# Performance work log

Measured on AMD Instinct MI355X. Metric: run time of the kernel, lower is better.

## Reference

```python
import jax, jax.numpy as jnp
import numpy as np
import math

B, E, N = 32, 256, 64
KV_DIM, Q_DIM = 100, 768


def setup_inputs() -> dict:
    key = jax.random.key(0)
    ks = jax.random.split(key, 8)
    q = jax.random.normal(ks[0], (B, Q_DIM), dtype=jnp.float32)
    k = jax.random.normal(ks[1], (B, E, N, KV_DIM), dtype=jnp.float32)
    v = jax.random.normal(ks[2], (B, E, N, KV_DIM), dtype=jnp.float32)
    input_ent = jax.random.randint(ks[3], (B, E), 0, 50000)
    # xavier-uniform-initialized weights (torch Linear: y = x @ W.T + b)
    def xavier(k_, fan_out, fan_in):
        lim = math.sqrt(6.0 / (fan_in + fan_out))
        return jax.random.uniform(k_, (fan_out, fan_in), jnp.float32, -lim, lim)
    W_q = xavier(ks[4], KV_DIM, Q_DIM)
    b_q = jnp.zeros((KV_DIM,), jnp.float32)
    W_kv = xavier(ks[5], KV_DIM, KV_DIM)
    W_v = xavier(ks[6], KV_DIM, KV_DIM)
    return {"input_ent": input_ent, "q": q, "k": k, "v": v,
            "W_q": W_q, "b_q": b_q, "W_kv": W_kv, "W_v": W_v}


def reference(input_ent, q, k, v, W_q, b_q, W_kv, W_v):
    # mode == 'candidate_pos', graphsage=False -> output = self_attention(q, k, v)
    # Q projection + tanh: [B, Kv]
    Qp = jnp.tanh(q @ W_q.T + b_q)
    # K projection: [B, E, N, Kv]
    Kp = k @ W_kv.T
    # broadcasted dot-product score: [B, E, N]
    att = jnp.einsum('bd,bend->ben', Qp, Kp) / math.sqrt(KV_DIM)
    # masked_fill(att == 0, -10000)
    att = jnp.where(att == 0.0, jnp.float32(-10000.0), att)
    # LeakyReLU (default negative_slope=0.01) then softmax over neighbor dim
    att = jax.nn.softmax(jax.nn.leaky_relu(att, 0.01), axis=2)
    # masked_fill(att == 1/N, 0)
    att = jnp.where(att == jnp.float32(1.0 / N), jnp.float32(0.0), att)
    # V projection and weighted aggregation over neighbors: [B, E, Kv]
    Vp = v @ W_v.T
    return jnp.einsum('ben,bend->bed', att, Vp)
```

## Files before the change

### kernel.cpp

```cpp
#include <hip/hip_runtime.h>

#define B 32
#define E 256
#define N 64
#define KV 100
#define QD 768

__global__ __launch_bounds__(256) void prep_kernel(
    const float* __restrict__ q,
    const float* __restrict__ W_q,
    const float* __restrict__ b_q,
    const float* __restrict__ W_kv,
    const float* __restrict__ W_v,
    float* __restrict__ Qk,
    float* __restrict__ W_vT)
{
    const int blk = blockIdx.x;
    const int tid = threadIdx.x;

    if (blk == B) {
        for (int idx = tid; idx < KV * KV; idx += 256) {
            int d = idx / KV, i = idx % KV;
            W_vT[idx] = W_v[i * KV + d];
        }
        return;
    }

    __shared__ float q_lds[QD];
    __shared__ float Qp_lds[KV];
    const int b = blk;

    for (int i = tid; i < QD; i += 256) q_lds[i] = q[b * QD + i];
    __syncthreads();

    const int i = tid >> 1, h = tid & 1;
    if (i < KV) {
        float acc = 0.f;
        const float* wrow = W_q + i * QD + h * (QD / 2);
        const float* qrow = q_lds + h * (QD / 2);
        #pragma unroll 8
        for (int d = 0; d < QD / 2; d++) acc += qrow[d] * wrow[d];
        acc += __shfl_xor(acc, 1);
        if (h == 0) Qp_lds[i] = tanhf(acc + b_q[i]);
    }
    __syncthreads();

    if (tid < KV) {
        float acc = 0.f;
        #pragma unroll 4
        for (int ii = 0; ii < KV; ii++) acc += Qp_lds[ii] * W_kv[ii * KV + tid];
        Qk[b * KV + tid] = acc * 0.1f;
    }
}

__global__ __launch_bounds__(256) void attn_kernel(
    const float* __restrict__ k,
    const float* __restrict__ v,
    const float* __restrict__ Qk,
    const float* __restrict__ W_vT,
    float* __restrict__ out)
{
    __shared__ float att_lds[N];
    __shared__ float part_lds[2][KV];
    __shared__ float agg_lds[KV];

    const int tid = threadIdx.x;
    const int be  = blockIdx.x;
    const int b   = be >> 8;

    {
        const int n = tid >> 2, sub = tid & 3;
        const float4* krow = (const float4*)(k + (size_t)be * (N * KV) + n * KV);
        const float4* qk4  = (const float4*)(Qk + b * KV);
        float acc = 0.f;
        #pragma unroll
        for (int j = sub; j < KV / 4; j += 4) {
            float4 kk = krow[j];
            float4 qq = qk4[j];
            acc += qq.x * kk.x + qq.y * kk.y + qq.z * kk.z + qq.w * kk.w;
        }
        acc += __shfl_xor(acc, 1);
        acc += __shfl_xor(acc, 2);
        if (sub == 0) {
            float a = acc;
            if (a == 0.0f) a = -10000.0f;
            a = (a > 0.0f) ? a : 0.01f * a;
            att_lds[n] = a;
        }
    }
    __syncthreads();

    if (tid < 64) {
        float x = att_lds[tid];
        float m = x;
        #pragma unroll
        for (int o = 32; o; o >>= 1) m = fmaxf(m, __shfl_xor(m, o));
        float e = __expf(x - m);
        float s = e;
        #pragma unroll
        for (int o = 32; o; o >>= 1) s += __shfl_xor(s, o);
        float r = e / s;
        if (r == 0.015625f) r = 0.0f;
        att_lds[tid] = r;
    }
    __syncthreads();

    if (tid < 200) {
        const int half = tid / 100;
        const int d    = tid - half * 100;
        const float* vcol = v + (size_t)be * (N * KV) + d;
        float a = 0.f;
        #pragma unroll
        for (int i = 0; i < 32; i++) {
            int nn = half * 32 + i;
            a += att_lds[nn] * vcol[(size_t)nn * KV];
        }
        part_lds[half][d] = a;
    }
    __syncthreads();

    if (tid < KV) agg_lds[tid] = part_lds[0][tid] + part_lds[1][tid];
    __syncthreads();

    if (tid < KV) {
        float acc = 0.f;
        #pragma unroll 4
        for (int d = 0; d < KV; d++)
            acc += agg_lds[d] * W_vT[d * KV + tid];
        out[(size_t)be * KV + tid] = acc;
    }
}

extern "C" void kernel_launch(void* const* d_in, const int* in_sizes, int n_in,
                              void* d_out, int out_size, void* d_ws, size_t ws_size,
                              hipStream_t stream) {
    const float* q    = (const float*)d_in[1];
    const float* k    = (const float*)d_in[2];
    const float* v    = (const float*)d_in[3];
    const float* W_q  = (const float*)d_in[4];
    const float* b_q  = (const float*)d_in[5];
    const float* W_kv = (const float*)d_in[6];
    const float* W_v  = (const float*)d_in[7];
    float* out  = (float*)d_out;

    float* Qk   = (float*)d_ws;
    float* W_vT = Qk + B * KV;

    prep_kernel<<<B + 1, 256, 0, stream>>>(q, W_q, b_q, W_kv, W_v, Qk, W_vT);
    attn_kernel<<<B * E, 256, 0, stream>>>(k, v, Qk, W_vT, out);
}
```

Baseline: 113.6 us.

## Split attention into score and aggregation kernels with vectorized V loads

Splits the fused attention kernel into a score kernel that streams K and writes raw scores to workspace, and an aggregation kernel. The aggregation kernel issues its float4 V register loads before the softmax so the V fetch overlaps the score reads and the reduction. The final projection now reads W_v rows directly as float4, which removes the W_v transpose from the prep kernel. This adds a third launch and a round trip of the score array through global memory.

```diff
diff --git a/kernel.cpp b/kernel.cpp
--- a/kernel.cpp
+++ b/kernel.cpp
@@ -11,24 +11,13 @@
     const float* __restrict__ W_q,
     const float* __restrict__ b_q,
     const float* __restrict__ W_kv,
-    const float* __restrict__ W_v,
-    float* __restrict__ Qk,
-    float* __restrict__ W_vT)
+    float* __restrict__ Qk)
 {
-    const int blk = blockIdx.x;
     const int tid = threadIdx.x;
-
-    if (blk == B) {
-        for (int idx = tid; idx < KV * KV; idx += 256) {
-            int d = idx / KV, i = idx % KV;
-            W_vT[idx] = W_v[i * KV + d];
-        }
-        return;
-    }
+    const int b   = blockIdx.x;
 
     __shared__ float q_lds[QD];
     __shared__ float Qp_lds[KV];
-    const int b = blk;
 
     for (int i = tid; i < QD; i += 256) q_lds[i] = q[b * QD + i];
     __syncthreads();
@@ -53,45 +42,62 @@
     }
 }
 
-__global__ __launch_bounds__(256) void attn_kernel(
+__global__ __launch_bounds__(256) void score_kernel(
     const float* __restrict__ k,
+    const float* __restrict__ Qk,
+    float* __restrict__ att_raw)
+{
+    const int tid  = threadIdx.x;
+    const int quad = tid >> 2, sub = tid & 3;
+    const int r    = blockIdx.x * 64 + quad;
+    const int b    = r >> 14;
+
+    const float4* krow = (const float4*)(k + (size_t)r * KV);
+    const float4* qk4  = (const float4*)(Qk + b * KV);
+
+    float acc = 0.f;
+    #pragma unroll
+    for (int j = sub; j < KV / 4; j += 4) {
+        float4 kk = krow[j];
+        float4 qq = qk4[j];
+        acc += qq.x * kk.x + qq.y * kk.y + qq.z * kk.z + qq.w * kk.w;
+    }
+    acc += __shfl_xor(acc, 1);
+    acc += __shfl_xor(acc, 2);
+    if (sub == 0) {
+        float a = acc;
+        if (a == 0.0f) a = -10000.0f;
+        a = (a > 0.0f) ? a : 0.01f * a;
+        att_raw[r] = a;
+    }
+}
+
+__global__ __launch_bounds__(256) void agg_kernel(
     const float* __restrict__ v,
-    const float* __restrict__ Qk,
-    const float* __restrict__ W_vT,
+    const float* __restrict__ att_raw,
+    const float* __restrict__ W_v,
     float* __restrict__ out)
 {
     __shared__ float att_lds[N];
-    __shared__ float part_lds[2][KV];
-    __shared__ float agg_lds[KV];
+    __shared__ __align__(16) float part_lds[8][KV];
+    __shared__ __align__(16) float agg_lds[KV];
 
     const int tid = threadIdx.x;
     const int be  = blockIdx.x;
-    const int b   = be >> 8;
 
-    {
-        const int n = tid >> 2, sub = tid & 3;
-        const float4* krow = (const float4*)(k + (size_t)be * (N * KV) + n * KV);
-        const float4* qk4  = (const float4*)(Qk + b * KV);
-        float acc = 0.f;
+    const bool active = tid < 200;
+    const int  c  = tid % 25;
+    const int  ng = tid / 25;
+    float4 vr[8];
+    if (active) {
+        const float4* vb = (const float4*)(v + (size_t)be * (N * KV));
         #pragma unroll
-        for (int j = sub; j < KV / 4; j += 4) {
-            float4 kk = krow[j];
-            float4 qq = qk4[j];
-            acc += qq.x * kk.x + qq.y * kk.y + qq.z * kk.z + qq.w * kk.w;
-        }
-        acc += __shfl_xor(acc, 1);
-        acc += __shfl_xor(acc, 2);
-        if (sub == 0) {
-            float a = acc;
-            if (a == 0.0f) a = -10000.0f;
-            a = (a > 0.0f) ? a : 0.01f * a;
-            att_lds[n] = a;
-        }
+        for (int i = 0; i < 8; i++)
+            vr[i] = vb[(ng * 8 + i) * (KV / 4) + c];
     }
-    __syncthreads();
 
     if (tid < 64) {
-        float x = att_lds[tid];
+        float x = att_raw[(size_t)be * N + tid];
         float m = x;
         #pragma unroll
         for (int o = 32; o; o >>= 1) m = fmaxf(m, __shfl_xor(m, o));
@@ -105,29 +111,41 @@
     }
     __syncthreads();
 
-    if (tid < 200) {
-        const int half = tid / 100;
-        const int d    = tid - half * 100;
-        const float* vcol = v + (size_t)be * (N * KV) + d;
-        float a = 0.f;
+    if (active) {
+        float4 a4 = make_float4(0.f, 0.f, 0.f, 0.f);
         #pragma unroll
-        for (int i = 0; i < 32; i++) {
-            int nn = half * 32 + i;
-            a += att_lds[nn] * vcol[(size_t)nn * KV];
+        for (int i = 0; i < 8; i++) {
+            float w = att_lds[ng * 8 + i];
+            a4.x += w * vr[i].x;
+            a4.y += w * vr[i].y;
+            a4.z += w * vr[i].z;
+            a4.w += w * vr[i].w;
         }
-        part_lds[half][d] = a;
+        *(float4*)&part_lds[ng][c * 4] = a4;
     }
     __syncthreads();
 
-    if (tid < KV) agg_lds[tid] = part_lds[0][tid] + part_lds[1][tid];
+    if (tid < KV) {
+        float s = 0.f;
+        #pragma unroll
+        for (int g = 0; g < 8; g++) s += part_lds[g][tid];
+        agg_lds[tid] = s;
+    }
     __syncthreads();
 
-    if (tid < KV) {
+    const int p = tid >> 1, h = tid & 1;
+    if (p < KV) {
+        const float4* wrow = (const float4*)(W_v + p * KV);
+        const float4* a4   = (const float4*)agg_lds;
         float acc = 0.f;
-        #pragma unroll 4
-        for (int d = 0; d < KV; d++)
-            acc += agg_lds[d] * W_vT[d * KV + tid];
-        out[(size_t)be * KV + tid] = acc;
+        #pragma unroll
+        for (int j = h; j < KV / 4; j += 2) {
+            float4 w = wrow[j];
+            float4 a = a4[j];
+            acc += w.x * a.x + w.y * a.y + w.z * a.z + w.w * a.w;
+        }
+        acc += __shfl_xor(acc, 1);
+        if (h == 0) out[(size_t)be * KV + p] = acc;
     }
 }
 
@@ -143,9 +161,10 @@
     const float* W_v  = (const float*)d_in[7];
     float* out  = (float*)d_out;
 
-    float* Qk   = (float*)d_ws;
-    float* W_vT = Qk + B * KV;
+    float* Qk      = (float*)d_ws;
+    float* att_raw = Qk + B * KV;
 
-    prep_kernel<<<B + 1, 256, 0, stream>>>(q, W_q, b_q, W_kv, W_v, Qk, W_vT);
-    attn_kernel<<<B * E, 256, 0, stream>>>(k, v, Qk, W_vT, out);
+    prep_kernel<<<B, 256, 0, stream>>>(q, W_q, b_q, W_kv, Qk);
+    score_kernel<<<(B * E * N) / 64, 256, 0, stream>>>(k, Qk, att_raw);
+    agg_kernel<<<B * E, 256, 0, stream>>>(v, att_raw, W_v, out);
 }
```

New measurement: 144.6 us. 1.27x slower.

## Map one (b,e) attention row per wavefront and drop block barriers

Applied to the files above, without the earlier changes.

Restructures the attention kernel so each 64-lane wavefront handles one (b,e) pair, with four pairs per block. All __syncthreads are removed, and softmax is computed directly in registers from per-lane row dot products. The V aggregation now uses float4 loads with a parity split combined by shuffle. The output projection reads W_v rows with float4 directly, which removes the transpose work in the prep kernel. The trade-off is that per-lane K row reads are strided (each lane reads its own 400-byte row), which may hurt coalescing, and the loads are serialized within each wave.

```diff
diff --git a/kernel.cpp b/kernel.cpp
--- a/kernel.cpp
+++ b/kernel.cpp
@@ -5,30 +5,20 @@
 #define N 64
 #define KV 100
 #define QD 768
+#define WAVES 4
 
 __global__ __launch_bounds__(256) void prep_kernel(
     const float* __restrict__ q,
     const float* __restrict__ W_q,
     const float* __restrict__ b_q,
     const float* __restrict__ W_kv,
-    const float* __restrict__ W_v,
-    float* __restrict__ Qk,
-    float* __restrict__ W_vT)
+    float* __restrict__ Qk)
 {
-    const int blk = blockIdx.x;
     const int tid = threadIdx.x;
-
-    if (blk == B) {
-        for (int idx = tid; idx < KV * KV; idx += 256) {
-            int d = idx / KV, i = idx % KV;
-            W_vT[idx] = W_v[i * KV + d];
-        }
-        return;
-    }
+    const int b   = blockIdx.x;
 
     __shared__ float q_lds[QD];
     __shared__ float Qp_lds[KV];
-    const int b = blk;
 
     for (int i = tid; i < QD; i += 256) q_lds[i] = q[b * QD + i];
     __syncthreads();
@@ -57,77 +47,93 @@
     const float* __restrict__ k,
     const float* __restrict__ v,
     const float* __restrict__ Qk,
-    const float* __restrict__ W_vT,
+    const float* __restrict__ W_v,
     float* __restrict__ out)
 {
-    __shared__ float att_lds[N];
-    __shared__ float part_lds[2][KV];
-    __shared__ float agg_lds[KV];
+    __shared__ __align__(16) float qk_lds[WAVES][KV];
+    __shared__ float att_lds[WAVES][N];
+    __shared__ __align__(16) float agg_lds[WAVES][KV];
 
-    const int tid = threadIdx.x;
-    const int be  = blockIdx.x;
-    const int b   = be >> 8;
+    const int tid  = threadIdx.x;
+    const int wid  = tid >> 6;
+    const int lane = tid & 63;
+    const int be   = blockIdx.x * WAVES + wid;
+    const int b    = be >> 8;
+
+    const float4* kbase = (const float4*)(k + (size_t)be * (N * KV));
+    const float4* vbase = (const float4*)(v + (size_t)be * (N * KV));
+
+    if (lane < KV / 4)
+        ((float4*)qk_lds[wid])[lane] = ((const float4*)(Qk + b * KV))[lane];
 
     {
-        const int n = tid >> 2, sub = tid & 3;
-        const float4* krow = (const float4*)(k + (size_t)be * (N * KV) + n * KV);
-        const float4* qk4  = (const float4*)(Qk + b * KV);
+        const float4* krow = kbase + lane * (KV / 4);
+        const float4* qq4  = (const float4*)qk_lds[wid];
         float acc = 0.f;
         #pragma unroll
-        for (int j = sub; j < KV / 4; j += 4) {
+        for (int j = 0; j < KV / 4; j++) {
             float4 kk = krow[j];
-            float4 qq = qk4[j];
+            float4 qq = qq4[j];
             acc += qq.x * kk.x + qq.y * kk.y + qq.z * kk.z + qq.w * kk.w;
         }
-        acc += __shfl_xor(acc, 1);
-        acc += __shfl_xor(acc, 2);
-        if (sub == 0) {
-            float a = acc;
-            if (a == 0.0f) a = -10000.0f;
-            a = (a > 0.0f) ? a : 0.01f * a;
-            att_lds[n] = a;
-        }
-    }
-    __syncthreads();
-
-    if (tid < 64) {
-        float x = att_lds[tid];
-        float m = x;
+        float a = acc;
+        if (a == 0.0f) a = -10000.0f;
+        a = (a > 0.0f) ? a : 0.01f * a;
+        float m = a;
         #pragma unroll
         for (int o = 32; o; o >>= 1) m = fmaxf(m, __shfl_xor(m, o));
-        float e = __expf(x - m);
+        float e = __expf(a - m);
         float s = e;
         #pragma unroll
         for (int o = 32; o; o >>= 1) s += __shfl_xor(s, o);
         float r = e / s;
-        if (r == 0.015625f) r = 0.0f;
-        att_lds[tid] = r;
+        if (r == 0.015625f) r = 0.f;
+        att_lds[wid][lane] = r;
     }
-    __syncthreads();
 
-    if (tid < 200) {
-        const int half = tid / 100;
-        const int d    = tid - half * 100;
-        const float* vcol = v + (size_t)be * (N * KV) + d;
-        float a = 0.f;
+    {
+        const int c   = (lane < 25) ? lane : lane - 25;
+        const int par = (lane < 25) ? 0 : 1;
+        float4 acc4 = make_float4(0.f, 0.f, 0.f, 0.f);
+        if (lane < 50) {
+            #pragma unroll
+            for (int i = 0; i < N / 2; i++) {
+                const int n = 2 * i + par;
+                float4 vv = vbase[n * (KV / 4) + c];
+                float  w  = att_lds[wid][n];
+                acc4.x += w * vv.x;
+                acc4.y += w * vv.y;
+                acc4.z += w * vv.z;
+                acc4.w += w * vv.w;
+            }
+        }
+        float ox = __shfl(acc4.x, lane + 25);
+        float oy = __shfl(acc4.y, lane + 25);
+        float oz = __shfl(acc4.z, lane + 25);
+        float ow = __shfl(acc4.w, lane + 25);
+        if (lane < 25) {
+            acc4.x += ox; acc4.y += oy; acc4.z += oz; acc4.w += ow;
+            ((float4*)agg_lds[wid])[lane] = acc4;
+        }
+    }
+
+    {
+        const float4* wv4 = (const float4*)W_v;
+        const float4* a4  = (const float4*)agg_lds[wid];
         #pragma unroll
-        for (int i = 0; i < 32; i++) {
-            int nn = half * 32 + i;
-            a += att_lds[nn] * vcol[(size_t)nn * KV];
+        for (int p = 0; p < 2; p++) {
+            const int i = p * 64 + lane;
+            if (i < KV) {
+                float acc = 0.f;
+                #pragma unroll
+                for (int j = 0; j < KV / 4; j++) {
+                    float4 w = wv4[i * (KV / 4) + j];
+                    float4 a = a4[j];
+                    acc += w.x * a.x + w.y * a.y + w.z * a.z + w.w * a.w;
+                }
+                out[(size_t)be * KV + i] = acc;
+            }
         }
-        part_lds[half][d] = a;
-    }
-    __syncthreads();
-
-    if (tid < KV) agg_lds[tid] = part_lds[0][tid] + part_lds[1][tid];
-    __syncthreads();
-
-    if (tid < KV) {
-        float acc = 0.f;
-        #pragma unroll 4
-        for (int d = 0; d < KV; d++)
-            acc += agg_lds[d] * W_vT[d * KV + tid];
-        out[(size_t)be * KV + tid] = acc;
     }
 }
 
@@ -143,9 +149,8 @@
     const float* W_v  = (const float*)d_in[7];
     float* out  = (float*)d_out;
 
-    float* Qk   = (float*)d_ws;
-    float* W_vT = Qk + B * KV;
+    float* Qk = (float*)d_ws;
 
-    prep_kernel<<<B + 1, 256, 0, stream>>>(q, W_q, b_q, W_kv, W_v, Qk, W_vT);
-    attn_kernel<<<B * E, 256, 0, stream>>>(k, v, Qk, W_vT, out);
+    prep_kernel<<<B, 256, 0, stream>>>(q, W_q, b_q, W_kv, Qk);
+    attn_kernel<<<(B * E) / WAVES, 256, 0, stream>>>(k, v, Qk, W_v, out);
 }
```

After: 147.5 us. +29.8%, slower.

## Async-prefetch V into LDS and split V projection into separate kernel

Applied to the files above, without the earlier changes.

The attention kernel now issues all K loads into registers up front and streams the whole V tile into LDS with asynchronous global-to-LDS loads, so V traffic overlaps the score and softmax phases. The final W_v projection moves out into a new per-wavefront kernel that reads W_v directly with float4 loads, which removes the W_v transpose block from prep. The aim is to hide memory latency in the bandwidth-bound attention pass. The cost is a third launch, an extra round trip of the aggregated vectors through global memory, and about 25KB of LDS per block, which limits occupancy.

```diff
diff --git a/kernel.cpp b/kernel.cpp
--- a/kernel.cpp
+++ b/kernel.cpp
@@ -6,29 +6,25 @@
 #define KV 100
 #define QD 768
 
+#define ASYNC16(gsrc, ldst) \
+    __builtin_amdgcn_global_load_lds( \
+        (const __attribute__((address_space(1))) void*)(gsrc), \
+        (__attribute__((address_space(3))) void*)(ldst), 16, 0, 0)
+
+__device__ __forceinline__ float dot4f(float4 a, float4 b) {
+    return a.x * b.x + a.y * b.y + a.z * b.z + a.w * b.w;
+}
+
 __global__ __launch_bounds__(256) void prep_kernel(
-    const float* __restrict__ q,
-    const float* __restrict__ W_q,
-    const float* __restrict__ b_q,
-    const float* __restrict__ W_kv,
-    const float* __restrict__ W_v,
-    float* __restrict__ Qk,
-    float* __restrict__ W_vT)
+    const float* __restrict__ q, const float* __restrict__ W_q,
+    const float* __restrict__ b_q, const float* __restrict__ W_kv,
+    float* __restrict__ Qk)
 {
-    const int blk = blockIdx.x;
     const int tid = threadIdx.x;
-
-    if (blk == B) {
-        for (int idx = tid; idx < KV * KV; idx += 256) {
-            int d = idx / KV, i = idx % KV;
-            W_vT[idx] = W_v[i * KV + d];
-        }
-        return;
-    }
+    const int b   = blockIdx.x;
 
     __shared__ float q_lds[QD];
     __shared__ float Qp_lds[KV];
-    const int b = blk;
 
     for (int i = tid; i < QD; i += 256) q_lds[i] = q[b * QD + i];
     __syncthreads();
@@ -53,31 +49,53 @@
     }
 }
 
-__global__ __launch_bounds__(256) void attn_kernel(
+__global__ __launch_bounds__(256, 6) void attn_kernel(
     const float* __restrict__ k,
     const float* __restrict__ v,
     const float* __restrict__ Qk,
-    const float* __restrict__ W_vT,
-    float* __restrict__ out)
+    float* __restrict__ agg_out)
 {
+    __shared__ __align__(16) float vbuf[N * KV];
     __shared__ float att_lds[N];
-    __shared__ float part_lds[2][KV];
-    __shared__ float agg_lds[KV];
 
-    const int tid = threadIdx.x;
-    const int be  = blockIdx.x;
-    const int b   = be >> 8;
+    const int tid  = threadIdx.x;
+    const int wid  = tid >> 6;
+    const int lane = tid & 63;
+    const int be   = blockIdx.x;
+    const int b    = be >> 8;
+
+    const float4* kb4  = (const float4*)(k + (size_t)be * (N * KV));
+    const float4* vb4  = (const float4*)(v + (size_t)be * (N * KV));
+    const float4* qk4g = (const float4*)(Qk + b * KV);
+    float4* vbuf4 = (float4*)vbuf;
+
+    const int n = tid >> 2, sub = tid & 3;
+    const float4* krow = kb4 + n * (KV / 4);
+
+    float4 kk[7], qq[7];
+    #pragma unroll
+    for (int i = 0; i < 7; i++) {
+        int j = sub + 4 * i; if (j > 24) j = 24;
+        kk[i] = krow[j];
+    }
+    #pragma unroll
+    for (int i = 0; i < 7; i++) {
+        int j = sub + 4 * i; if (j > 24) j = 24;
+        qq[i] = qk4g[j];
+    }
+    #pragma unroll
+    for (int t = 0; t < 6; t++) {
+        const int c = wid + 4 * t;
+        ASYNC16(vb4 + c * 64 + lane, vbuf4 + c * 64);
+    }
+    ASYNC16(vb4 + 24 * 64 + lane, vbuf4 + 24 * 64);
 
     {
-        const int n = tid >> 2, sub = tid & 3;
-        const float4* krow = (const float4*)(k + (size_t)be * (N * KV) + n * KV);
-        const float4* qk4  = (const float4*)(Qk + b * KV);
         float acc = 0.f;
         #pragma unroll
-        for (int j = sub; j < KV / 4; j += 4) {
-            float4 kk = krow[j];
-            float4 qq = qk4[j];
-            acc += qq.x * kk.x + qq.y * kk.y + qq.z * kk.z + qq.w * kk.w;
+        for (int i = 0; i < 7; i++) {
+            float g = (sub + 4 * i <= 24) ? 1.f : 0.f;
+            acc += g * dot4f(kk[i], qq[i]);
         }
         acc += __shfl_xor(acc, 1);
         acc += __shfl_xor(acc, 2);
@@ -100,34 +118,43 @@
         #pragma unroll
         for (int o = 32; o; o >>= 1) s += __shfl_xor(s, o);
         float r = e / s;
-        if (r == 0.015625f) r = 0.0f;
+        if (r == 0.015625f) r = 0.f;
         att_lds[tid] = r;
     }
     __syncthreads();
 
-    if (tid < 200) {
-        const int half = tid / 100;
-        const int d    = tid - half * 100;
-        const float* vcol = v + (size_t)be * (N * KV) + d;
+    if (tid < KV) {
         float a = 0.f;
-        #pragma unroll
-        for (int i = 0; i < 32; i++) {
-            int nn = half * 32 + i;
-            a += att_lds[nn] * vcol[(size_t)nn * KV];
+        #pragma unroll 8
+        for (int nn = 0; nn < N; nn++)
+            a += att_lds[nn] * vbuf[nn * KV + tid];
+        agg_out[(size_t)be * KV + tid] = a;
+    }
+}
+
+__global__ __launch_bounds__(256) void proj_kernel(
+    const float* __restrict__ agg,
+    const float* __restrict__ W_v,
+    float* __restrict__ out)
+{
+    __shared__ __align__(16) float a_lds[4][KV];
+    const int tid = threadIdx.x, wid = tid >> 6, lane = tid & 63;
+    const int be  = blockIdx.x * 4 + wid;
+
+    if (lane < 25)
+        ((float4*)a_lds[wid])[lane] = ((const float4*)(agg + (size_t)be * KV))[lane];
+
+    const float4* wv4 = (const float4*)W_v;
+    const float4* a4  = (const float4*)a_lds[wid];
+    #pragma unroll
+    for (int p = 0; p < 2; p++) {
+        const int i = p * 64 + lane;
+        if (i < KV) {
+            float acc = 0.f;
+            #pragma unroll
+            for (int j = 0; j < 25; j++) acc += dot4f(wv4[i * 25 + j], a4[j]);
+            out[(size_t)be * KV + i] = acc;
         }
-        part_lds[half][d] = a;
-    }
-    __syncthreads();
-
-    if (tid < KV) agg_lds[tid] = part_lds[0][tid] + part_lds[1][tid];
-    __syncthreads();
-
-    if (tid < KV) {
-        float acc = 0.f;
-        #pragma unroll 4
-        for (int d = 0; d < KV; d++)
-            acc += agg_lds[d] * W_vT[d * KV + tid];
-        out[(size_t)be * KV + tid] = acc;
     }
 }
 
@@ -143,9 +170,10 @@
     const float* W_v  = (const float*)d_in[7];
     float* out  = (float*)d_out;
 
-    float* Qk   = (float*)d_ws;
-    float* W_vT = Qk + B * KV;
+    float* Qk  = (float*)d_ws;
+    float* agg = Qk + B * KV;
 
-    prep_kernel<<<B + 1, 256, 0, stream>>>(q, W_q, b_q, W_kv, W_v, Qk, W_vT);
-    attn_kernel<<<B * E, 256, 0, stream>>>(k, v, Qk, W_vT, out);
+    prep_kernel<<<B, 256, 0, stream>>>(q, W_q, b_q, W_kv, Qk);
+    attn_kernel<<<B * E, 256, 0, stream>>>(k, v, Qk, agg);
+    proj_kernel<<<(B * E) / 4, 256, 0, stream>>>(agg, W_v, out);
 }
```

Result: slower. 127.1 us (+11.8%).
